# Kernel tuning notes

Hardware: AMD Instinct MI355X
Metric: run time of the kernel (lower is better)

The kernel has to match this reference:

```python
import jax, jax.numpy as jnp
import numpy as np

K = 3  # from init kwarg


def setup_inputs() -> dict:
    key = jax.random.key(0)
    k1, k2 = jax.random.split(key)
    B, N, D = 32, 2048, 128
    features = jax.random.normal(k1, (B, N, D), dtype=jnp.float32)
    strength = jax.random.uniform(k2, (), dtype=jnp.float32)
    return {"features": features, "strength": strength}


def reference(features, strength):
    B, N, D = features.shape
    k = min(K, N - 1)
    x = jax.lax.stop_gradient(features)  # torch uses features.detach() for the mix path

    # pairwise euclidean distance (torch.cdist, p=2): ||a||^2 + ||b||^2 - 2 a.b
    sq = jnp.sum(x * x, axis=-1)                     # (B, N)
    d2 = sq[:, :, None] + sq[:, None, :] - 2.0 * jnp.einsum('bnd,bmd->bnm', x, x)
    dist = jnp.sqrt(jnp.maximum(d2, 0.0))            # (B, N, N)

    # mask self-distance with +1e6 on the diagonal
    eye = jnp.eye(N, dtype=dist.dtype)
    dist = dist + eye[None, :, :] * 1000000.0

    # k smallest -> top_k of negated distances
    _, idx = jax.lax.top_k(-dist, k)                 # idx: (B, N, k)

    # gather neighbor features: gathered[b,n,j] = x[b, idx[b,n,j]]
    gathered = x[jnp.arange(B)[:, None, None], idx]  # (B, N, k, D)
    mix = jnp.mean(gathered, axis=2)                 # (B, N, D)

    s = jnp.clip(strength, 0.0, 1.0)
    return (1.0 - s) * features + s * mix
```

## Files before the change

kernel.cpp:

```cpp
#include <hip/hip_runtime.h>
#include <cfloat>

#define BB 32
#define NN 2048
#define DD 128
#define RM 128
#define CN 64

typedef __attribute__((ext_vector_type(8))) short short8;
typedef __attribute__((ext_vector_type(4))) short short4v;
typedef __attribute__((ext_vector_type(4))) float float4v;

__device__ __forceinline__ unsigned short f2bf(float f) {
    unsigned int u = __builtin_bit_cast(unsigned int, f);
    u += 0x7FFFu + ((u >> 16) & 1u);
    return (unsigned short)(u >> 16);
}

__device__ __forceinline__ unsigned int umn(unsigned int a, unsigned int b) { return a < b ? a : b; }
__device__ __forceinline__ unsigned int umx(unsigned int a, unsigned int b) { return a > b ? a : b; }
#define CSU(a, b) { unsigned int _lo = umn(a, b), _hi = umx(a, b); (a) = _lo; (b) = _hi; }

__device__ __forceinline__ unsigned int umed3(unsigned int a, unsigned int b, unsigned int c) {
    unsigned int d;
    asm("v_med3_u32 %0, %1, %2, %3" : "=v"(d) : "v"(a), "v"(b), "v"(c));
    return d;
}

__device__ __forceinline__ void gl2lds16(const unsigned short* g, unsigned short* l) {
    __builtin_amdgcn_global_load_lds(
        (const __attribute__((address_space(1))) void*)g,
        (__attribute__((address_space(3))) void*)l, 16, 0, 0);
}

__global__ __launch_bounds__(256) void prep_kernel(const float* __restrict__ x,
        unsigned short* __restrict__ xb16, float* __restrict__ sq) {
    int c = blockIdx.x * 256 + threadIdx.x;
    float4 v = *reinterpret_cast<const float4*>(x + (size_t)c * 4);
    short4v pk;
    pk[0] = (short)f2bf(v.x); pk[1] = (short)f2bf(v.y);
    pk[2] = (short)f2bf(v.z); pk[3] = (short)f2bf(v.w);
    *reinterpret_cast<short4v*>(xb16 + (size_t)c * 4) = pk;
    float acc = v.x * v.x + v.y * v.y + v.z * v.z + v.w * v.w;
    acc += __shfl_xor(acc, 1);
    acc += __shfl_xor(acc, 2);
    acc += __shfl_xor(acc, 4);
    acc += __shfl_xor(acc, 8);
    acc += __shfl_xor(acc, 16);
    if ((threadIdx.x & 31) == 0) sq[c >> 5] = acc;
}

__global__ __launch_bounds__(256) void sq_kernel(const float* __restrict__ x,
                                                 float* __restrict__ sq) {
    int t = blockIdx.x * 256 + threadIdx.x;
    int row = t >> 2;
    int q = t & 3;
    const float4* xp = reinterpret_cast<const float4*>(x + (size_t)row * DD + q * 32);
    float acc = 0.f;
#pragma unroll
    for (int i = 0; i < 8; ++i) {
        float4 v = xp[i];
        acc += v.x * v.x + v.y * v.y + v.z * v.z + v.w * v.w;
    }
    acc += __shfl_xor(acc, 1);
    acc += __shfl_xor(acc, 2);
    if (q == 0) sq[row] = acc;
}

template<bool PRE>
__global__ __launch_bounds__(256, 2) void knn_kernel(const float* __restrict__ x,
        const unsigned short* __restrict__ xb16g,
        const float* __restrict__ sqv, const float* __restrict__ strength,
        float* __restrict__ out) {
    __shared__ __align__(16) unsigned short btile[2 * CN * DD];
    __shared__ unsigned int cand8[RM * 8];

    const int b = blockIdx.x;
    const int row0 = blockIdx.y * RM;
    const int tid = threadIdx.x;
    const int w = tid >> 6;
    const int lane = tid & 63;
    const int m = lane & 15;
    const int quad = lane >> 4;
    const float* __restrict__ xb = x + (size_t)b * NN * DD;
    const unsigned short* __restrict__ gb = PRE ? xb16g + (size_t)b * NN * DD : nullptr;

    short8 afrag[2][4];
    if constexpr (PRE) {
#pragma unroll
        for (int rg = 0; rg < 2; ++rg)
#pragma unroll
            for (int kc = 0; kc < 4; ++kc)
                afrag[rg][kc] = *reinterpret_cast<const short8*>(
                    gb + (size_t)(row0 + 32 * w + rg * 16 + m) * DD + kc * 32 + quad * 8);
    } else {
#pragma unroll
        for (int rg = 0; rg < 2; ++rg)
#pragma unroll
            for (int kc = 0; kc < 4; ++kc) {
                const float4* src = reinterpret_cast<const float4*>(
                    xb + (size_t)(row0 + 32 * w + rg * 16 + m) * DD + kc * 32 + quad * 8);
                float4 v0 = src[0], v1 = src[1];
                short8 pk;
                pk[0] = (short)f2bf(v0.x); pk[1] = (short)f2bf(v0.y);
                pk[2] = (short)f2bf(v0.z); pk[3] = (short)f2bf(v0.w);
                pk[4] = (short)f2bf(v1.x); pk[5] = (short)f2bf(v1.y);
                pk[6] = (short)f2bf(v1.z); pk[7] = (short)f2bf(v1.w);
                afrag[rg][kc] = pk;
            }
    }

    {
        unsigned short* buf = btile;
        if constexpr (PRE) {
#pragma unroll
            for (int l = 0; l < 4; ++l) {
                int f = (l * 4 + w) * 64 + lane;
                int r = f >> 4, p = f & 15;
                int c = p ^ (r & 7);
                gl2lds16(gb + (size_t)r * DD + c * 8, buf + (l * 4 + w) * 512);
            }
        } else {
#pragma unroll
            for (int l = 0; l < 4; ++l) {
                int id = l * 256 + tid;
                int r = id >> 4, c = id & 15, p = c ^ (r & 7);
                const float4* src = reinterpret_cast<const float4*>(xb + (size_t)r * DD + c * 8);
                float4 v0 = src[0], v1 = src[1];
                short8 pk;
                pk[0] = (short)f2bf(v0.x); pk[1] = (short)f2bf(v0.y);
                pk[2] = (short)f2bf(v0.z); pk[3] = (short)f2bf(v0.w);
                pk[4] = (short)f2bf(v1.x); pk[5] = (short)f2bf(v1.y);
                pk[6] = (short)f2bf(v1.z); pk[7] = (short)f2bf(v1.w);
                *reinterpret_cast<short8*>(buf + r * DD + p * 8) = pk;
            }
        }
    }
    __syncthreads();

    unsigned int tk[2][4][4];
#pragma unroll
    for (int rg = 0; rg < 2; ++rg)
#pragma unroll
        for (int i = 0; i < 4; ++i)
#pragma unroll
            for (int q = 0; q < 4; ++q) tk[rg][i][q] = 0xFFFFFFFFu;

    for (int ct = 0; ct < NN / CN; ++ct) {
        unsigned short* cur = btile + (size_t)(ct & 1) * CN * DD;
        unsigned short* nxt = btile + (size_t)((ct + 1) & 1) * CN * DD;

        if (ct + 1 < NN / CN) {
            int cb = (ct + 1) * CN;
            if constexpr (PRE) {
#pragma unroll
                for (int l = 0; l < 4; ++l) {
                    int f = (l * 4 + w) * 64 + lane;
                    int r = f >> 4, p = f & 15;
                    int c = p ^ (r & 7);
                    gl2lds16(gb + (size_t)(cb + r) * DD + c * 8, nxt + (l * 4 + w) * 512);
                }
            } else {
#pragma unroll
                for (int l = 0; l < 4; ++l) {
                    int id = l * 256 + tid;
                    int r = id >> 4, c = id & 15, p = c ^ (r & 7);
                    const float4* src = reinterpret_cast<const float4*>(xb + (size_t)(cb + r) * DD + c * 8);
                    float4 v0 = src[0], v1 = src[1];
                    short8 pk;
                    pk[0] = (short)f2bf(v0.x); pk[1] = (short)f2bf(v0.y);
                    pk[2] = (short)f2bf(v0.z); pk[3] = (short)f2bf(v0.w);
                    pk[4] = (short)f2bf(v1.x); pk[5] = (short)f2bf(v1.y);
                    pk[6] = (short)f2bf(v1.z); pk[7] = (short)f2bf(v1.w);
                    *reinterpret_cast<short8*>(nxt + r * DD + p * 8) = pk;
                }
            }
        }

        float sqb[4];
#pragma unroll
        for (int cc = 0; cc < 4; ++cc)
            sqb[cc] = sqv[(size_t)b * NN + ct * CN + cc * 16 + m] + 1024.0f;

        float4v acc[2][4];
#pragma unroll
        for (int rg = 0; rg < 2; ++rg)
#pragma unroll
            for (int cc = 0; cc < 4; ++cc) acc[rg][cc] = (float4v){0.f, 0.f, 0.f, 0.f};
        __builtin_amdgcn_s_setprio(1);
#pragma unroll
        for (int kc = 0; kc < 4; ++kc) {
            short8 bfrag[4];
#pragma unroll
            for (int cc = 0; cc < 4; ++cc) {
                int rl = cc * 16 + m;
                int p = (kc * 4 + quad) ^ (m & 7);
                bfrag[cc] = *reinterpret_cast<const short8*>(cur + rl * DD + p * 8);
            }
#pragma unroll
            for (int rg = 0; rg < 2; ++rg)
#pragma unroll
                for (int cc = 0; cc < 4; ++cc)
                    acc[rg][cc] = __builtin_amdgcn_mfma_f32_16x16x32_bf16(
                        afrag[rg][kc], bfrag[cc], acc[rg][cc], 0, 0, 0);
        }
        __builtin_amdgcn_s_setprio(0);

#pragma unroll
        for (int cc = 0; cc < 4; ++cc) {
            unsigned int col = (unsigned int)(ct * CN + cc * 16 + m);
#pragma unroll
            for (int rg = 0; rg < 2; ++rg)
#pragma unroll
                for (int reg = 0; reg < 4; ++reg) {
                    float scb = fmaf(-2.f, acc[rg][cc][reg], sqb[cc]);
                    unsigned int key = (__builtin_bit_cast(unsigned int, scb) & 0xFFFFF800u) | col;
                    unsigned int t0 = tk[rg][reg][0], t1 = tk[rg][reg][1];
                    unsigned int t2 = tk[rg][reg][2], t3 = tk[rg][reg][3];
                    tk[rg][reg][0] = umn(t0, key);
                    tk[rg][reg][1] = umed3(t0, t1, key);
                    tk[rg][reg][2] = umed3(t1, t2, key);
                    tk[rg][reg][3] = umed3(t2, t3, key);
                }
        }

        __syncthreads();
    }

#pragma unroll
    for (int rg = 0; rg < 2; ++rg)
#pragma unroll
        for (int reg = 0; reg < 4; ++reg) {
            unsigned int e[8];
#pragma unroll
            for (int j = 0; j < 4; ++j) e[j] = tk[rg][reg][j];
#pragma unroll
            for (int j = 4; j < 8; ++j) e[j] = 0xFFFFFFFFu;
#pragma unroll
            for (int st = 0; st < 4; ++st) {
                int mask = 1 << st;
                unsigned int rv[8];
#pragma unroll
                for (int j = 0; j < 8; ++j)
                    rv[j] = (unsigned int)__shfl_xor((int)e[7 - j], mask, 64);
#pragma unroll
                for (int j = 0; j < 8; ++j) e[j] = umn(e[j], rv[j]);
                CSU(e[0], e[4]); CSU(e[1], e[5]); CSU(e[2], e[6]); CSU(e[3], e[7]);
                CSU(e[0], e[2]); CSU(e[1], e[3]); CSU(e[4], e[6]); CSU(e[5], e[7]);
                CSU(e[0], e[1]); CSU(e[2], e[3]); CSU(e[4], e[5]); CSU(e[6], e[7]);
            }
            if (m == 0) {
                int row = 32 * w + rg * 16 + quad * 4 + reg;
#pragma unroll
                for (int j = 0; j < 8; ++j) cand8[row * 8 + j] = e[j];
            }
        }
    __syncthreads();

    double* refd = reinterpret_cast<double*>(btile);
    int* best3 = reinterpret_cast<int*>(btile) + 2048;

    {
        int r = tid >> 1, h = tid & 1;
        int grow = row0 + r;
        int ci[4];
#pragma unroll
        for (int j = 0; j < 4; ++j) ci[j] = (int)(cand8[r * 8 + h * 4 + j] & 0x7FFu);
        const float* pr = xb + (size_t)grow * DD;
        const float* pc[4];
#pragma unroll
        for (int j = 0; j < 4; ++j) pc[j] = xb + (size_t)ci[j] * DD;
        double a[4] = {0.0, 0.0, 0.0, 0.0};
#pragma unroll 4
        for (int d4 = 0; d4 < 32; ++d4) {
            float4 wv = *reinterpret_cast<const float4*>(pr + d4 * 4);
#pragma unroll
            for (int j = 0; j < 4; ++j) {
                float4 v = *reinterpret_cast<const float4*>(pc[j] + d4 * 4);
                double d;
                d = (double)wv.x - (double)v.x; a[j] += d * d;
                d = (double)wv.y - (double)v.y; a[j] += d * d;
                d = (double)wv.z - (double)v.z; a[j] += d * d;
                d = (double)wv.w - (double)v.w; a[j] += d * d;
            }
        }
#pragma unroll
        for (int j = 0; j < 4; ++j)
            refd[r * 8 + h * 4 + j] = (ci[j] == grow) ? DBL_MAX : a[j];
    }
    __syncthreads();

    if (tid < RM) {
        int r = tid;
        double b0 = DBL_MAX, b1 = DBL_MAX, b2 = DBL_MAX;
        int i0 = 0x7fffffff, i1 = 0x7fffffff, i2 = 0x7fffffff;
        for (int e = 0; e < 8; ++e) {
            double dv = refd[r * 8 + e];
            int ix = (int)(cand8[r * 8 + e] & 0x7FFu);
            if (dv < b2 || (dv == b2 && ix < i2)) {
                b2 = dv; i2 = ix;
                if (b1 > b2 || (b1 == b2 && i1 > i2)) { double td = b1; b1 = b2; b2 = td; int tn = i1; i1 = i2; i2 = tn; }
                if (b0 > b1 || (b0 == b1 && i0 > i1)) { double td = b0; b0 = b1; b1 = td; int tn = i0; i0 = i1; i1 = tn; }
            }
        }
        best3[r * 3 + 0] = i0; best3[r * 3 + 1] = i1; best3[r * 3 + 2] = i2;
    }
    __syncthreads();

    {
        int r = tid >> 1, q = tid & 1;
        float s = fminf(fmaxf(strength[0], 0.f), 1.f);
        const float* pa = xb + (size_t)(row0 + r) * DD + q * 64;
        const float* p1 = xb + (size_t)best3[r * 3 + 0] * DD + q * 64;
        const float* p2 = xb + (size_t)best3[r * 3 + 1] * DD + q * 64;
        const float* p3 = xb + (size_t)best3[r * 3 + 2] * DD + q * 64;
        float* po = out + ((size_t)b * NN + row0 + r) * DD + q * 64;
#pragma unroll
        for (int l = 0; l < 16; ++l) {
            float4 a  = *reinterpret_cast<const float4*>(pa + l * 4);
            float4 n1 = *reinterpret_cast<const float4*>(p1 + l * 4);
            float4 n2 = *reinterpret_cast<const float4*>(p2 + l * 4);
            float4 n3 = *reinterpret_cast<const float4*>(p3 + l * 4);
            float4 o;
            o.x = (1.f - s) * a.x + s * ((n1.x + n2.x + n3.x) / 3.f);
            o.y = (1.f - s) * a.y + s * ((n1.y + n2.y + n3.y) / 3.f);
            o.z = (1.f - s) * a.z + s * ((n1.z + n2.z + n3.z) / 3.f);
            o.w = (1.f - s) * a.w + s * ((n1.w + n2.w + n3.w) / 3.f);
            *reinterpret_cast<float4*>(po + l * 4) = o;
        }
    }
}

extern "C" void kernel_launch(void* const* d_in, const int* in_sizes, int n_in,
                              void* d_out, int out_size, void* d_ws, size_t ws_size,
                              hipStream_t stream) {
    const float* x = (const float*)d_in[0];
    const float* strength = (const float*)d_in[1];
    float* out = (float*)d_out;
    float* sq = (float*)d_ws;
    unsigned short* xb16 = (unsigned short*)((char*)d_ws + 256 * 1024);
    const size_t need = 256 * 1024 + (size_t)BB * NN * DD * sizeof(unsigned short);

    if (ws_size >= need) {
        prep_kernel<<<dim3((BB * NN * DD / 4) / 256), 256, 0, stream>>>(x, xb16, sq);
        knn_kernel<true><<<dim3(BB, NN / RM), 256, 0, stream>>>(x, xb16, sq, strength, out);
    } else {
        sq_kernel<<<dim3((BB * NN * 4) / 256), 256, 0, stream>>>(x, sq);
        knn_kernel<false><<<dim3(BB, NN / RM), 256, 0, stream>>>(x, nullptr, sq, strength, out);
    }
}
```

Before: 193.4 us.

## Split KNN column range across two blocks and merge partial top-3 in new kernel

The distance/top-k kernel now runs over half of the candidate columns per block (grid z=2), doubling the block count. Each half writes its refined top-3 distances and indices as scratch into the output buffer. A new merge kernel combines the two partial lists and computes the final mix. Launch bounds rise to 4 waves per SIMD and the setprio hints are removed, trading an extra launch and scratch traffic for more parallelism and occupancy.

```diff
diff --git a/kernel.cpp b/kernel.cpp
--- a/kernel.cpp
+++ b/kernel.cpp
@@ -6,6 +6,8 @@
 #define DD 128
 #define RM 128
 #define CN 64
+#define NH (NN / 2)
+#define NITERH (NH / CN)
 
 typedef __attribute__((ext_vector_type(8))) short short8;
 typedef __attribute__((ext_vector_type(4))) short short4v;
@@ -68,15 +70,16 @@
 }
 
 template<bool PRE>
-__global__ __launch_bounds__(256, 2) void knn_kernel(const float* __restrict__ x,
+__global__ __launch_bounds__(256, 4) void knn_half(const float* __restrict__ x,
         const unsigned short* __restrict__ xb16g,
-        const float* __restrict__ sqv, const float* __restrict__ strength,
-        float* __restrict__ out) {
+        const float* __restrict__ sqv, float* __restrict__ out) {
     __shared__ __align__(16) unsigned short btile[2 * CN * DD];
     __shared__ unsigned int cand8[RM * 8];
 
     const int b = blockIdx.x;
     const int row0 = blockIdx.y * RM;
+    const int h = blockIdx.z;
+    const int cbase = h * NH;
     const int tid = threadIdx.x;
     const int w = tid >> 6;
     const int lane = tid & 63;
@@ -118,14 +121,14 @@
                 int f = (l * 4 + w) * 64 + lane;
                 int r = f >> 4, p = f & 15;
                 int c = p ^ (r & 7);
-                gl2lds16(gb + (size_t)r * DD + c * 8, buf + (l * 4 + w) * 512);
+                gl2lds16(gb + (size_t)(cbase + r) * DD + c * 8, buf + (l * 4 + w) * 512);
             }
         } else {
 #pragma unroll
             for (int l = 0; l < 4; ++l) {
                 int id = l * 256 + tid;
                 int r = id >> 4, c = id & 15, p = c ^ (r & 7);
-                const float4* src = reinterpret_cast<const float4*>(xb + (size_t)r * DD + c * 8);
+                const float4* src = reinterpret_cast<const float4*>(xb + (size_t)(cbase + r) * DD + c * 8);
                 float4 v0 = src[0], v1 = src[1];
                 short8 pk;
                 pk[0] = (short)f2bf(v0.x); pk[1] = (short)f2bf(v0.y);
@@ -146,12 +149,12 @@
 #pragma unroll
             for (int q = 0; q < 4; ++q) tk[rg][i][q] = 0xFFFFFFFFu;
 
-    for (int ct = 0; ct < NN / CN; ++ct) {
+    for (int ct = 0; ct < NITERH; ++ct) {
         unsigned short* cur = btile + (size_t)(ct & 1) * CN * DD;
         unsigned short* nxt = btile + (size_t)((ct + 1) & 1) * CN * DD;
 
-        if (ct + 1 < NN / CN) {
-            int cb = (ct + 1) * CN;
+        if (ct + 1 < NITERH) {
+            int cb = cbase + (ct + 1) * CN;
             if constexpr (PRE) {
 #pragma unroll
                 for (int l = 0; l < 4; ++l) {
@@ -180,14 +183,13 @@
         float sqb[4];
 #pragma unroll
         for (int cc = 0; cc < 4; ++cc)
-            sqb[cc] = sqv[(size_t)b * NN + ct * CN + cc * 16 + m] + 1024.0f;
+            sqb[cc] = sqv[(size_t)b * NN + cbase + ct * CN + cc * 16 + m] + 1024.0f;
 
         float4v acc[2][4];
 #pragma unroll
         for (int rg = 0; rg < 2; ++rg)
 #pragma unroll
             for (int cc = 0; cc < 4; ++cc) acc[rg][cc] = (float4v){0.f, 0.f, 0.f, 0.f};
-        __builtin_amdgcn_s_setprio(1);
 #pragma unroll
         for (int kc = 0; kc < 4; ++kc) {
             short8 bfrag[4];
@@ -204,11 +206,10 @@
                     acc[rg][cc] = __builtin_amdgcn_mfma_f32_16x16x32_bf16(
                         afrag[rg][kc], bfrag[cc], acc[rg][cc], 0, 0, 0);
         }
-        __builtin_amdgcn_s_setprio(0);
 
 #pragma unroll
         for (int cc = 0; cc < 4; ++cc) {
-            unsigned int col = (unsigned int)(ct * CN + cc * 16 + m);
+            unsigned int col = (unsigned int)(cbase + ct * CN + cc * 16 + m);
 #pragma unroll
             for (int rg = 0; rg < 2; ++rg)
 #pragma unroll
@@ -258,14 +259,13 @@
     __syncthreads();
 
     double* refd = reinterpret_cast<double*>(btile);
-    int* best3 = reinterpret_cast<int*>(btile) + 2048;
 
     {
-        int r = tid >> 1, h = tid & 1;
+        int r = tid >> 1, hh = tid & 1;
         int grow = row0 + r;
         int ci[4];
 #pragma unroll
-        for (int j = 0; j < 4; ++j) ci[j] = (int)(cand8[r * 8 + h * 4 + j] & 0x7FFu);
+        for (int j = 0; j < 4; ++j) ci[j] = (int)(cand8[r * 8 + hh * 4 + j] & 0x7FFu);
         const float* pr = xb + (size_t)grow * DD;
         const float* pc[4];
 #pragma unroll
@@ -286,7 +286,7 @@
         }
 #pragma unroll
         for (int j = 0; j < 4; ++j)
-            refd[r * 8 + h * 4 + j] = (ci[j] == grow) ? DBL_MAX : a[j];
+            refd[r * 8 + hh * 4 + j] = (ci[j] == grow) ? DBL_MAX : a[j];
     }
     __syncthreads();
 
@@ -303,31 +303,61 @@
                 if (b0 > b1 || (b0 == b1 && i0 > i1)) { double td = b0; b0 = b1; b1 = td; int tn = i0; i0 = i1; i1 = tn; }
             }
         }
-        best3[r * 3 + 0] = i0; best3[r * 3 + 1] = i1; best3[r * 3 + 2] = i2;
-    }
-    __syncthreads();
-
-    {
-        int r = tid >> 1, q = tid & 1;
-        float s = fminf(fmaxf(strength[0], 0.f), 1.f);
-        const float* pa = xb + (size_t)(row0 + r) * DD + q * 64;
-        const float* p1 = xb + (size_t)best3[r * 3 + 0] * DD + q * 64;
-        const float* p2 = xb + (size_t)best3[r * 3 + 1] * DD + q * 64;
-        const float* p3 = xb + (size_t)best3[r * 3 + 2] * DD + q * 64;
-        float* po = out + ((size_t)b * NN + row0 + r) * DD + q * 64;
-#pragma unroll
-        for (int l = 0; l < 16; ++l) {
-            float4 a  = *reinterpret_cast<const float4*>(pa + l * 4);
-            float4 n1 = *reinterpret_cast<const float4*>(p1 + l * 4);
-            float4 n2 = *reinterpret_cast<const float4*>(p2 + l * 4);
-            float4 n3 = *reinterpret_cast<const float4*>(p3 + l * 4);
-            float4 o;
-            o.x = (1.f - s) * a.x + s * ((n1.x + n2.x + n3.x) / 3.f);
-            o.y = (1.f - s) * a.y + s * ((n1.y + n2.y + n3.y) / 3.f);
-            o.z = (1.f - s) * a.z + s * ((n1.z + n2.z + n3.z) / 3.f);
-            o.w = (1.f - s) * a.w + s * ((n1.w + n2.w + n3.w) / 3.f);
-            *reinterpret_cast<float4*>(po + l * 4) = o;
-        }
+        float* scr = out + ((size_t)b * NN + row0 + r) * DD + h * 16;
+        double* sd = reinterpret_cast<double*>(scr);
+        sd[0] = b0; sd[1] = b1; sd[2] = b2;
+        int* si = reinterpret_cast<int*>(scr + 6);
+        si[0] = i0; si[1] = i1; si[2] = i2;
+    }
+}
+
+__global__ __launch_bounds__(256) void merge_out(const float* __restrict__ x,
+        const float* __restrict__ strength, float* __restrict__ out) {
+    int t = blockIdx.x * 256 + threadIdx.x;
+    int rgl = t >> 1, q = t & 1;
+    int b = rgl >> 11;
+    const float* xb = x + (size_t)b * NN * DD;
+    int r = rgl & (NN - 1);
+    float* row_out = out + (size_t)rgl * DD;
+
+    double d[6]; int ix[6];
+#pragma unroll
+    for (int h = 0; h < 2; ++h) {
+        const double* sd = reinterpret_cast<const double*>(row_out + h * 16);
+        const int* si = reinterpret_cast<const int*>(row_out + h * 16 + 6);
+#pragma unroll
+        for (int j = 0; j < 3; ++j) { d[h * 3 + j] = sd[j]; ix[h * 3 + j] = si[j]; }
+    }
+    double b0 = DBL_MAX, b1 = DBL_MAX, b2 = DBL_MAX;
+    int i0 = 0x7fffffff, i1 = 0x7fffffff, i2 = 0x7fffffff;
+#pragma unroll
+    for (int e = 0; e < 6; ++e) {
+        double dv = d[e]; int iv = ix[e];
+        if (dv < b2 || (dv == b2 && iv < i2)) {
+            b2 = dv; i2 = iv;
+            if (b1 > b2 || (b1 == b2 && i1 > i2)) { double td = b1; b1 = b2; b2 = td; int tn = i1; i1 = i2; i2 = tn; }
+            if (b0 > b1 || (b0 == b1 && i0 > i1)) { double td = b0; b0 = b1; b1 = td; int tn = i0; i0 = i1; i1 = tn; }
+        }
+    }
+    (void)r;
+    float s = fminf(fmaxf(strength[0], 0.f), 1.f);
+    const float* pa = xb + (size_t)(rgl & (NN - 1)) * DD + q * 64;
+    const float* p1 = xb + (size_t)i0 * DD + q * 64;
+    const float* p2 = xb + (size_t)i1 * DD + q * 64;
+    const float* p3 = xb + (size_t)i2 * DD + q * 64;
+    float* po = row_out + q * 64;
+#pragma unroll
+    for (int l = 0; l < 16; ++l) {
+        float4 a  = *reinterpret_cast<const float4*>(pa + l * 4);
+        float4 n1 = *reinterpret_cast<const float4*>(p1 + l * 4);
+        float4 n2 = *reinterpret_cast<const float4*>(p2 + l * 4);
+        float4 n3 = *reinterpret_cast<const float4*>(p3 + l * 4);
+        float4 o;
+        o.x = (1.f - s) * a.x + s * ((n1.x + n2.x + n3.x) / 3.f);
+        o.y = (1.f - s) * a.y + s * ((n1.y + n2.y + n3.y) / 3.f);
+        o.z = (1.f - s) * a.z + s * ((n1.z + n2.z + n3.z) / 3.f);
+        o.w = (1.f - s) * a.w + s * ((n1.w + n2.w + n3.w) / 3.f);
+        *reinterpret_cast<float4*>(po + l * 4) = o;
     }
 }
 
@@ -343,9 +373,10 @@
 
     if (ws_size >= need) {
         prep_kernel<<<dim3((BB * NN * DD / 4) / 256), 256, 0, stream>>>(x, xb16, sq);
-        knn_kernel<true><<<dim3(BB, NN / RM), 256, 0, stream>>>(x, xb16, sq, strength, out);
+        knn_half<true><<<dim3(BB, NN / RM, 2), 256, 0, stream>>>(x, xb16, sq, out);
     } else {
         sq_kernel<<<dim3((BB * NN * 4) / 256), 256, 0, stream>>>(x, sq);
-        knn_kernel<false><<<dim3(BB, NN / RM), 256, 0, stream>>>(x, nullptr, sq, strength, out);
-    }
-}
+        knn_half<false><<<dim3(BB, NN / RM, 2), 256, 0, stream>>>(x, nullptr, sq, out);
+    }
+    merge_out<<<dim3((BB * NN * 2) / 256), 256, 0, stream>>>(x, strength, out);
+}
```

Result: slower. 276.9 us (+43.2%).

## Fuse bf16 conversion and norm computation into single kNN kernel with register-staged prefetch

Applied to the files above, without the earlier changes.

Removes the separate prep kernel that wrote a bf16 copy of the features and their squared norms. The kNN kernel now reads fp32 tiles directly, converts them with the packed v_cvt_pk_bf16_f32 instruction, and computes squared norms on the fly into a small LDS buffer. Next-tile global loads are staged in registers before the MFMA work and written to LDS after the top-k update, which overlaps memory latency with compute. It also drops the setprio hints. The cost is redundant conversion and norm work in every block (16 row-blocks per batch), twice the global read bytes of fp32 versus bf16, and extra register pressure from the staged loads.

```diff
diff --git a/kernel.cpp b/kernel.cpp
--- a/kernel.cpp
+++ b/kernel.cpp
@@ -6,16 +6,10 @@
 #define DD 128
 #define RM 128
 #define CN 64
+#define NT (NN / CN)
 
 typedef __attribute__((ext_vector_type(8))) short short8;
-typedef __attribute__((ext_vector_type(4))) short short4v;
 typedef __attribute__((ext_vector_type(4))) float float4v;
-
-__device__ __forceinline__ unsigned short f2bf(float f) {
-    unsigned int u = __builtin_bit_cast(unsigned int, f);
-    u += 0x7FFFu + ((u >> 16) & 1u);
-    return (unsigned short)(u >> 16);
-}
 
 __device__ __forceinline__ unsigned int umn(unsigned int a, unsigned int b) { return a < b ? a : b; }
 __device__ __forceinline__ unsigned int umx(unsigned int a, unsigned int b) { return a > b ? a : b; }
@@ -27,53 +21,23 @@
     return d;
 }
 
-__device__ __forceinline__ void gl2lds16(const unsigned short* g, unsigned short* l) {
-    __builtin_amdgcn_global_load_lds(
-        (const __attribute__((address_space(1))) void*)g,
-        (__attribute__((address_space(3))) void*)l, 16, 0, 0);
-}
-
-__global__ __launch_bounds__(256) void prep_kernel(const float* __restrict__ x,
-        unsigned short* __restrict__ xb16, float* __restrict__ sq) {
-    int c = blockIdx.x * 256 + threadIdx.x;
-    float4 v = *reinterpret_cast<const float4*>(x + (size_t)c * 4);
-    short4v pk;
-    pk[0] = (short)f2bf(v.x); pk[1] = (short)f2bf(v.y);
-    pk[2] = (short)f2bf(v.z); pk[3] = (short)f2bf(v.w);
-    *reinterpret_cast<short4v*>(xb16 + (size_t)c * 4) = pk;
-    float acc = v.x * v.x + v.y * v.y + v.z * v.z + v.w * v.w;
-    acc += __shfl_xor(acc, 1);
-    acc += __shfl_xor(acc, 2);
-    acc += __shfl_xor(acc, 4);
-    acc += __shfl_xor(acc, 8);
-    acc += __shfl_xor(acc, 16);
-    if ((threadIdx.x & 31) == 0) sq[c >> 5] = acc;
-}
-
-__global__ __launch_bounds__(256) void sq_kernel(const float* __restrict__ x,
-                                                 float* __restrict__ sq) {
-    int t = blockIdx.x * 256 + threadIdx.x;
-    int row = t >> 2;
-    int q = t & 3;
-    const float4* xp = reinterpret_cast<const float4*>(x + (size_t)row * DD + q * 32);
-    float acc = 0.f;
-#pragma unroll
-    for (int i = 0; i < 8; ++i) {
-        float4 v = xp[i];
-        acc += v.x * v.x + v.y * v.y + v.z * v.z + v.w * v.w;
-    }
-    acc += __shfl_xor(acc, 1);
-    acc += __shfl_xor(acc, 2);
-    if (q == 0) sq[row] = acc;
-}
-
-template<bool PRE>
-__global__ __launch_bounds__(256, 2) void knn_kernel(const float* __restrict__ x,
-        const unsigned short* __restrict__ xb16g,
-        const float* __restrict__ sqv, const float* __restrict__ strength,
-        float* __restrict__ out) {
+__device__ __forceinline__ unsigned int cvtpk(float lo, float hi) {
+    unsigned int r;
+    asm("v_cvt_pk_bf16_f32 %0, %1, %2" : "=v"(r) : "v"(lo), "v"(hi));
+    return r;
+}
+__device__ __forceinline__ short8 pk8(float4 a, float4 b) {
+    union { unsigned int u[4]; short8 s; } z;
+    z.u[0] = cvtpk(a.x, a.y); z.u[1] = cvtpk(a.z, a.w);
+    z.u[2] = cvtpk(b.x, b.y); z.u[3] = cvtpk(b.z, b.w);
+    return z.s;
+}
+
+__global__ __launch_bounds__(256, 2) void knn_fused(const float* __restrict__ x,
+        const float* __restrict__ strength, float* __restrict__ out) {
     __shared__ __align__(16) unsigned short btile[2 * CN * DD];
     __shared__ unsigned int cand8[RM * 8];
+    __shared__ float sql[2][CN];
 
     const int b = blockIdx.x;
     const int row0 = blockIdx.y * RM;
@@ -83,111 +47,73 @@
     const int m = lane & 15;
     const int quad = lane >> 4;
     const float* __restrict__ xb = x + (size_t)b * NN * DD;
-    const unsigned short* __restrict__ gb = PRE ? xb16g + (size_t)b * NN * DD : nullptr;
 
     short8 afrag[2][4];
-    if constexpr (PRE) {
-#pragma unroll
-        for (int rg = 0; rg < 2; ++rg)
-#pragma unroll
-            for (int kc = 0; kc < 4; ++kc)
-                afrag[rg][kc] = *reinterpret_cast<const short8*>(
-                    gb + (size_t)(row0 + 32 * w + rg * 16 + m) * DD + kc * 32 + quad * 8);
-    } else {
-#pragma unroll
-        for (int rg = 0; rg < 2; ++rg)
-#pragma unroll
-            for (int kc = 0; kc < 4; ++kc) {
-                const float4* src = reinterpret_cast<const float4*>(
-                    xb + (size_t)(row0 + 32 * w + rg * 16 + m) * DD + kc * 32 + quad * 8);
-                float4 v0 = src[0], v1 = src[1];
-                short8 pk;
-                pk[0] = (short)f2bf(v0.x); pk[1] = (short)f2bf(v0.y);
-                pk[2] = (short)f2bf(v0.z); pk[3] = (short)f2bf(v0.w);
-                pk[4] = (short)f2bf(v1.x); pk[5] = (short)f2bf(v1.y);
-                pk[6] = (short)f2bf(v1.z); pk[7] = (short)f2bf(v1.w);
-                afrag[rg][kc] = pk;
-            }
-    }
+#pragma unroll
+    for (int rg = 0; rg < 2; ++rg)
+#pragma unroll
+        for (int kc = 0; kc < 4; ++kc) {
+            const float4* src = reinterpret_cast<const float4*>(
+                xb + (size_t)(row0 + 32 * w + rg * 16 + m) * DD + kc * 32 + quad * 8);
+            afrag[rg][kc] = pk8(src[0], src[1]);
+        }
 
     {
-        unsigned short* buf = btile;
-        if constexpr (PRE) {
-#pragma unroll
-            for (int l = 0; l < 4; ++l) {
-                int f = (l * 4 + w) * 64 + lane;
-                int r = f >> 4, p = f & 15;
-                int c = p ^ (r & 7);
-                gl2lds16(gb + (size_t)r * DD + c * 8, buf + (l * 4 + w) * 512);
-            }
-        } else {
+#pragma unroll
+        for (int l = 0; l < 4; ++l) {
+            int id = l * 256 + tid;
+            int r = id >> 4, c = id & 15, p = c ^ (r & 7);
+            const float4* src = reinterpret_cast<const float4*>(xb + (size_t)r * DD + c * 8);
+            float4 v0 = src[0], v1 = src[1];
+            *reinterpret_cast<short8*>(btile + r * DD + p * 8) = pk8(v0, v1);
+            float ss = v0.x * v0.x + v0.y * v0.y + v0.z * v0.z + v0.w * v0.w
+                     + v1.x * v1.x + v1.y * v1.y + v1.z * v1.z + v1.w * v1.w;
+            ss += __shfl_xor(ss, 1);
+            ss += __shfl_xor(ss, 2);
+            ss += __shfl_xor(ss, 4);
+            ss += __shfl_xor(ss, 8);
+            if (c == 0) sql[0][r] = ss;
+        }
+    }
+    __syncthreads();
+
+    unsigned int tk[2][4][4];
+#pragma unroll
+    for (int rg = 0; rg < 2; ++rg)
+#pragma unroll
+        for (int i = 0; i < 4; ++i)
+#pragma unroll
+            for (int q = 0; q < 4; ++q) tk[rg][i][q] = 0xFFFFFFFFu;
+
+    for (int ct = 0; ct < NT; ++ct) {
+        unsigned short* cur = btile + (size_t)(ct & 1) * CN * DD;
+        unsigned short* nxt = btile + (size_t)((ct + 1) & 1) * CN * DD;
+        const bool pf = (ct + 1 < NT);
+
+        float4 st0[4], st1[4];
+        if (pf) {
+            int cb = (ct + 1) * CN;
 #pragma unroll
             for (int l = 0; l < 4; ++l) {
                 int id = l * 256 + tid;
-                int r = id >> 4, c = id & 15, p = c ^ (r & 7);
-                const float4* src = reinterpret_cast<const float4*>(xb + (size_t)r * DD + c * 8);
-                float4 v0 = src[0], v1 = src[1];
-                short8 pk;
-                pk[0] = (short)f2bf(v0.x); pk[1] = (short)f2bf(v0.y);
-                pk[2] = (short)f2bf(v0.z); pk[3] = (short)f2bf(v0.w);
-                pk[4] = (short)f2bf(v1.x); pk[5] = (short)f2bf(v1.y);
-                pk[6] = (short)f2bf(v1.z); pk[7] = (short)f2bf(v1.w);
-                *reinterpret_cast<short8*>(buf + r * DD + p * 8) = pk;
-            }
-        }
-    }
-    __syncthreads();
-
-    unsigned int tk[2][4][4];
-#pragma unroll
-    for (int rg = 0; rg < 2; ++rg)
-#pragma unroll
-        for (int i = 0; i < 4; ++i)
-#pragma unroll
-            for (int q = 0; q < 4; ++q) tk[rg][i][q] = 0xFFFFFFFFu;
-
-    for (int ct = 0; ct < NN / CN; ++ct) {
-        unsigned short* cur = btile + (size_t)(ct & 1) * CN * DD;
-        unsigned short* nxt = btile + (size_t)((ct + 1) & 1) * CN * DD;
-
-        if (ct + 1 < NN / CN) {
-            int cb = (ct + 1) * CN;
-            if constexpr (PRE) {
-#pragma unroll
-                for (int l = 0; l < 4; ++l) {
-                    int f = (l * 4 + w) * 64 + lane;
-                    int r = f >> 4, p = f & 15;
-                    int c = p ^ (r & 7);
-                    gl2lds16(gb + (size_t)(cb + r) * DD + c * 8, nxt + (l * 4 + w) * 512);
-                }
-            } else {
-#pragma unroll
-                for (int l = 0; l < 4; ++l) {
-                    int id = l * 256 + tid;
-                    int r = id >> 4, c = id & 15, p = c ^ (r & 7);
-                    const float4* src = reinterpret_cast<const float4*>(xb + (size_t)(cb + r) * DD + c * 8);
-                    float4 v0 = src[0], v1 = src[1];
-                    short8 pk;
-                    pk[0] = (short)f2bf(v0.x); pk[1] = (short)f2bf(v0.y);
-                    pk[2] = (short)f2bf(v0.z); pk[3] = (short)f2bf(v0.w);
-                    pk[4] = (short)f2bf(v1.x); pk[5] = (short)f2bf(v1.y);
-                    pk[6] = (short)f2bf(v1.z); pk[7] = (short)f2bf(v1.w);
-                    *reinterpret_cast<short8*>(nxt + r * DD + p * 8) = pk;
-                }
+                int r = id >> 4, c = id & 15;
+                const float4* src = reinterpret_cast<const float4*>(
+                    xb + (size_t)(cb + r) * DD + c * 8);
+                st0[l] = src[0];
+                st1[l] = src[1];
             }
         }
 
         float sqb[4];
 #pragma unroll
         for (int cc = 0; cc < 4; ++cc)
-            sqb[cc] = sqv[(size_t)b * NN + ct * CN + cc * 16 + m] + 1024.0f;
+            sqb[cc] = sql[ct & 1][cc * 16 + m] + 1024.0f;
 
         float4v acc[2][4];
 #pragma unroll
         for (int rg = 0; rg < 2; ++rg)
 #pragma unroll
             for (int cc = 0; cc < 4; ++cc) acc[rg][cc] = (float4v){0.f, 0.f, 0.f, 0.f};
-        __builtin_amdgcn_s_setprio(1);
 #pragma unroll
         for (int kc = 0; kc < 4; ++kc) {
             short8 bfrag[4];
@@ -204,7 +130,6 @@
                     acc[rg][cc] = __builtin_amdgcn_mfma_f32_16x16x32_bf16(
                         afrag[rg][kc], bfrag[cc], acc[rg][cc], 0, 0, 0);
         }
-        __builtin_amdgcn_s_setprio(0);
 
 #pragma unroll
         for (int cc = 0; cc < 4; ++cc) {
@@ -222,6 +147,24 @@
                     tk[rg][reg][2] = umed3(t1, t2, key);
                     tk[rg][reg][3] = umed3(t2, t3, key);
                 }
+        }
+
+        if (pf) {
+            float* sqn = sql[(ct + 1) & 1];
+#pragma unroll
+            for (int l = 0; l < 4; ++l) {
+                int id = l * 256 + tid;
+                int r = id >> 4, c = id & 15, p = c ^ (r & 7);
+                float4 v0 = st0[l], v1 = st1[l];
+                *reinterpret_cast<short8*>(nxt + r * DD + p * 8) = pk8(v0, v1);
+                float ss = v0.x * v0.x + v0.y * v0.y + v0.z * v0.z + v0.w * v0.w
+                         + v1.x * v1.x + v1.y * v1.y + v1.z * v1.z + v1.w * v1.w;
+                ss += __shfl_xor(ss, 1);
+                ss += __shfl_xor(ss, 2);
+                ss += __shfl_xor(ss, 4);
+                ss += __shfl_xor(ss, 8);
+                if (c == 0) sqn[r] = ss;
+            }
         }
 
         __syncthreads();
@@ -337,15 +280,7 @@
     const float* x = (const float*)d_in[0];
     const float* strength = (const float*)d_in[1];
     float* out = (float*)d_out;
-    float* sq = (float*)d_ws;
-    unsigned short* xb16 = (unsigned short*)((char*)d_ws + 256 * 1024);
-    const size_t need = 256 * 1024 + (size_t)BB * NN * DD * sizeof(unsigned short);
-
-    if (ws_size >= need) {
-        prep_kernel<<<dim3((BB * NN * DD / 4) / 256), 256, 0, stream>>>(x, xb16, sq);
-        knn_kernel<true><<<dim3(BB, NN / RM), 256, 0, stream>>>(x, xb16, sq, strength, out);
-    } else {
-        sq_kernel<<<dim3((BB * NN * 4) / 256), 256, 0, stream>>>(x, sq);
-        knn_kernel<false><<<dim3(BB, NN / RM), 256, 0, stream>>>(x, nullptr, sq, strength, out);
-    }
-}
+    (void)d_ws; (void)ws_size;
+
+    knn_fused<<<dim3(BB, NN / RM), 256, 0, stream>>>(x, strength, out);
+}
```

New measurement: 209.5 us. 1.08x slower.

## Split column tile across warp pairs, each warp covering 64 rows

Applied to the files above, without the earlier changes.

Changes the warp work split. Each pair of warps now shares 64 rows and each warp handles half of every 64-column tile, where before each warp handled 32 rows across all columns. The A fragments double and the B fragment LDS reads per warp halve, which cuts shared-memory traffic per MFMA. The cost is that each row now has two partial top-8 lists, so candidate count per row doubles to 16 and the fp64 refinement does twice the gather and distance work. The setprio hints around the MFMA loop are also removed, and register pressure rises from the larger afrag and tk arrays.

```diff
diff --git a/kernel.cpp b/kernel.cpp
--- a/kernel.cpp
+++ b/kernel.cpp
@@ -73,7 +73,7 @@
         const float* __restrict__ sqv, const float* __restrict__ strength,
         float* __restrict__ out) {
     __shared__ __align__(16) unsigned short btile[2 * CN * DD];
-    __shared__ unsigned int cand8[RM * 8];
+    __shared__ unsigned int cand16[RM * 16];
 
     const int b = blockIdx.x;
     const int row0 = blockIdx.y * RM;
@@ -82,24 +82,26 @@
     const int lane = tid & 63;
     const int m = lane & 15;
     const int quad = lane >> 4;
+    const int h = w >> 1;
+    const int cg = w & 1;
     const float* __restrict__ xb = x + (size_t)b * NN * DD;
     const unsigned short* __restrict__ gb = PRE ? xb16g + (size_t)b * NN * DD : nullptr;
 
-    short8 afrag[2][4];
+    short8 afrag[4][4];
     if constexpr (PRE) {
 #pragma unroll
-        for (int rg = 0; rg < 2; ++rg)
+        for (int rg = 0; rg < 4; ++rg)
 #pragma unroll
             for (int kc = 0; kc < 4; ++kc)
                 afrag[rg][kc] = *reinterpret_cast<const short8*>(
-                    gb + (size_t)(row0 + 32 * w + rg * 16 + m) * DD + kc * 32 + quad * 8);
+                    gb + (size_t)(row0 + h * 64 + rg * 16 + m) * DD + kc * 32 + quad * 8);
     } else {
 #pragma unroll
-        for (int rg = 0; rg < 2; ++rg)
+        for (int rg = 0; rg < 4; ++rg)
 #pragma unroll
             for (int kc = 0; kc < 4; ++kc) {
                 const float4* src = reinterpret_cast<const float4*>(
-                    xb + (size_t)(row0 + 32 * w + rg * 16 + m) * DD + kc * 32 + quad * 8);
+                    xb + (size_t)(row0 + h * 64 + rg * 16 + m) * DD + kc * 32 + quad * 8);
                 float4 v0 = src[0], v1 = src[1];
                 short8 pk;
                 pk[0] = (short)f2bf(v0.x); pk[1] = (short)f2bf(v0.y);
@@ -138,9 +140,9 @@
     }
     __syncthreads();
 
-    unsigned int tk[2][4][4];
-#pragma unroll
-    for (int rg = 0; rg < 2; ++rg)
+    unsigned int tk[4][4][4];
+#pragma unroll
+    for (int rg = 0; rg < 4; ++rg)
 #pragma unroll
         for (int i = 0; i < 4; ++i)
 #pragma unroll
@@ -177,40 +179,38 @@
             }
         }
 
-        float sqb[4];
-#pragma unroll
-        for (int cc = 0; cc < 4; ++cc)
-            sqb[cc] = sqv[(size_t)b * NN + ct * CN + cc * 16 + m] + 1024.0f;
-
-        float4v acc[2][4];
-#pragma unroll
-        for (int rg = 0; rg < 2; ++rg)
-#pragma unroll
-            for (int cc = 0; cc < 4; ++cc) acc[rg][cc] = (float4v){0.f, 0.f, 0.f, 0.f};
-        __builtin_amdgcn_s_setprio(1);
+        float sqb[2];
+#pragma unroll
+        for (int cc = 0; cc < 2; ++cc)
+            sqb[cc] = sqv[(size_t)b * NN + ct * CN + cg * 32 + cc * 16 + m] + 1024.0f;
+
+        float4v acc[4][2];
+#pragma unroll
+        for (int rg = 0; rg < 4; ++rg)
+#pragma unroll
+            for (int cc = 0; cc < 2; ++cc) acc[rg][cc] = (float4v){0.f, 0.f, 0.f, 0.f};
 #pragma unroll
         for (int kc = 0; kc < 4; ++kc) {
-            short8 bfrag[4];
-#pragma unroll
-            for (int cc = 0; cc < 4; ++cc) {
-                int rl = cc * 16 + m;
+            short8 bfrag[2];
+#pragma unroll
+            for (int cc = 0; cc < 2; ++cc) {
+                int rl = cg * 32 + cc * 16 + m;
                 int p = (kc * 4 + quad) ^ (m & 7);
                 bfrag[cc] = *reinterpret_cast<const short8*>(cur + rl * DD + p * 8);
             }
 #pragma unroll
-            for (int rg = 0; rg < 2; ++rg)
-#pragma unroll
-                for (int cc = 0; cc < 4; ++cc)
+            for (int rg = 0; rg < 4; ++rg)
+#pragma unroll
+                for (int cc = 0; cc < 2; ++cc)
                     acc[rg][cc] = __builtin_amdgcn_mfma_f32_16x16x32_bf16(
                         afrag[rg][kc], bfrag[cc], acc[rg][cc], 0, 0, 0);
         }
-        __builtin_amdgcn_s_setprio(0);
-
-#pragma unroll
-        for (int cc = 0; cc < 4; ++cc) {
-            unsigned int col = (unsigned int)(ct * CN + cc * 16 + m);
-#pragma unroll
-            for (int rg = 0; rg < 2; ++rg)
+
+#pragma unroll
+        for (int cc = 0; cc < 2; ++cc) {
+            unsigned int col = (unsigned int)(ct * CN + cg * 32 + cc * 16 + m);
+#pragma unroll
+            for (int rg = 0; rg < 4; ++rg)
 #pragma unroll
                 for (int reg = 0; reg < 4; ++reg) {
                     float scb = fmaf(-2.f, acc[rg][cc][reg], sqb[cc]);
@@ -228,7 +228,7 @@
     }
 
 #pragma unroll
-    for (int rg = 0; rg < 2; ++rg)
+    for (int rg = 0; rg < 4; ++rg)
 #pragma unroll
         for (int reg = 0; reg < 4; ++reg) {
             unsigned int e[8];
@@ -250,32 +250,32 @@
                 CSU(e[0], e[1]); CSU(e[2], e[3]); CSU(e[4], e[5]); CSU(e[6], e[7]);
             }
             if (m == 0) {
-                int row = 32 * w + rg * 16 + quad * 4 + reg;
-#pragma unroll
-                for (int j = 0; j < 8; ++j) cand8[row * 8 + j] = e[j];
+                int row = h * 64 + rg * 16 + quad * 4 + reg;
+#pragma unroll
+                for (int j = 0; j < 8; ++j) cand16[row * 16 + cg * 8 + j] = e[j];
             }
         }
     __syncthreads();
 
     double* refd = reinterpret_cast<double*>(btile);
-    int* best3 = reinterpret_cast<int*>(btile) + 2048;
+    int* best3 = reinterpret_cast<int*>(btile) + 4096;
 
     {
-        int r = tid >> 1, h = tid & 1;
+        int r = tid >> 1, hh = tid & 1;
         int grow = row0 + r;
-        int ci[4];
-#pragma unroll
-        for (int j = 0; j < 4; ++j) ci[j] = (int)(cand8[r * 8 + h * 4 + j] & 0x7FFu);
+        int ci[8];
+#pragma unroll
+        for (int j = 0; j < 8; ++j) ci[j] = (int)(cand16[r * 16 + hh * 8 + j] & 0x7FFu);
         const float* pr = xb + (size_t)grow * DD;
-        const float* pc[4];
-#pragma unroll
-        for (int j = 0; j < 4; ++j) pc[j] = xb + (size_t)ci[j] * DD;
-        double a[4] = {0.0, 0.0, 0.0, 0.0};
-#pragma unroll 4
+        const float* pc[8];
+#pragma unroll
+        for (int j = 0; j < 8; ++j) pc[j] = xb + (size_t)ci[j] * DD;
+        double a[8] = {0.0, 0.0, 0.0, 0.0, 0.0, 0.0, 0.0, 0.0};
+#pragma unroll 2
         for (int d4 = 0; d4 < 32; ++d4) {
             float4 wv = *reinterpret_cast<const float4*>(pr + d4 * 4);
 #pragma unroll
-            for (int j = 0; j < 4; ++j) {
+            for (int j = 0; j < 8; ++j) {
                 float4 v = *reinterpret_cast<const float4*>(pc[j] + d4 * 4);
                 double d;
                 d = (double)wv.x - (double)v.x; a[j] += d * d;
@@ -285,8 +285,8 @@
             }
         }
 #pragma unroll
-        for (int j = 0; j < 4; ++j)
-            refd[r * 8 + h * 4 + j] = (ci[j] == grow) ? DBL_MAX : a[j];
+        for (int j = 0; j < 8; ++j)
+            refd[r * 16 + hh * 8 + j] = (ci[j] == grow) ? DBL_MAX : a[j];
     }
     __syncthreads();
 
@@ -294,9 +294,9 @@
         int r = tid;
         double b0 = DBL_MAX, b1 = DBL_MAX, b2 = DBL_MAX;
         int i0 = 0x7fffffff, i1 = 0x7fffffff, i2 = 0x7fffffff;
-        for (int e = 0; e < 8; ++e) {
-            double dv = refd[r * 8 + e];
-            int ix = (int)(cand8[r * 8 + e] & 0x7FFu);
+        for (int e = 0; e < 16; ++e) {
+            double dv = refd[r * 16 + e];
+            int ix = (int)(cand16[r * 16 + e] & 0x7FFu);
             if (dv < b2 || (dv == b2 && ix < i2)) {
                 b2 = dv; i2 = ix;
                 if (b1 > b2 || (b1 == b2 && i1 > i2)) { double td = b1; b1 = b2; b2 = td; int tn = i1; i1 = i2; i2 = tn; }
```

After: 249.9 us. +29.2%, slower.
